# Performance work log

Hardware: AMD Instinct MI355X
Metric: run time of the kernel (lower is better)

## Reference

```python
import jax, jax.numpy as jnp
import numpy as np

N = 50000          # total residues (nodes)
E = 800000         # contact edges, avg degree 16
F_IN = 1280        # ESM embedding dim
H = 256            # hidden
L = 4              # num_layers
B = 100            # proteins in batch
MAX_NODES = 500    # residues per protein (uniform -> static to_dense_batch shape)


def setup_inputs() -> dict:
    key = jax.random.key(0)
    ks = jax.random.split(key, 16)
    s = 0.02
    inp = {
        "seq": jax.random.randint(ks[0], (N,), 0, 26),
        "edge_index": jax.random.randint(ks[1], (2, E), 0, N),
        "esm_token": jax.random.normal(ks[2], (N, F_IN), jnp.float32),
        "batch": jnp.arange(N) // MAX_NODES,
        # lin0
        "lin0_W": jax.random.normal(ks[3], (F_IN, H), jnp.float32) * s,
        "lin0_b": jnp.zeros((H,), jnp.float32),
        # WeightConv1 per layer: lin1 (root), lin2 (neighbor), lin3 (mask head)
        "wc_W1": jax.random.normal(ks[4], (L, H, H), jnp.float32) * s,
        "wc_b1": jnp.zeros((L, H), jnp.float32),
        "wc_W2": jax.random.normal(ks[5], (L, H, H), jnp.float32) * s,
        "wc_b2": jnp.zeros((L, H), jnp.float32),
        "wc_W3": jax.random.normal(ks[6], (L, H, H), jnp.float32) * s,
        "wc_b3": jnp.zeros((L, H), jnp.float32),
        # SparseConv per layer: neighbor weight + bias, root weight
        "sc_Wn": jax.random.normal(ks[7], (L, H, H), jnp.float32) * s,
        "sc_bn": jnp.zeros((L, H), jnp.float32),
        "sc_Wr": jax.random.normal(ks[8], (L, H, H), jnp.float32) * s,
    }
    return inp


def reference(seq, edge_index, esm_token, batch,
              lin0_W, lin0_b,
              wc_W1, wc_b1, wc_W2, wc_b2, wc_W3, wc_b3,
              sc_Wn, sc_bn, sc_Wr):
    src, dst = edge_index[0], edge_index[1]
    x = esm_token @ lin0_W + lin0_b              # [N, H]
    mask_val = None
    xs = []
    for i in range(L):
        # ---- WeightConv1: learned edge-conditioned node mask ----
        xm = x if mask_val is None else x * mask_val
        h_nb = xm @ wc_W2[i] + wc_b2[i]          # neighbor transform [N, H]
        agg = jax.ops.segment_sum(h_nb[src], dst, num_segments=N)
        h = jax.nn.relu(agg + xm @ wc_W1[i] + wc_b1[i])
        mask_val = jax.nn.sigmoid(h @ wc_W3[i] + wc_b3[i])   # [N, H]
        # ---- SparseConv: mask-gated sparse aggregation ----
        xg = x * mask_val
        agg2 = jax.ops.segment_sum(xg[src], dst, num_segments=N)
        x = jax.nn.relu(agg2 @ sc_Wn[i] + sc_bn[i] + x @ sc_Wr[i])
        xs.append(x)
    feat = jnp.concatenate(xs, axis=-1)          # jumping-knowledge cat [N, L*H]
    # ---- to_dense_batch ----
    counts = jax.ops.segment_sum(jnp.ones((N,), jnp.int32), batch, num_segments=B)
    starts = jnp.cumsum(counts) - counts
    pos = jnp.arange(N) - starts[batch]
    dense = jnp.zeros((B, MAX_NODES, L * H), feat.dtype).at[batch, pos].set(feat)
    node_mask = jnp.zeros((B, MAX_NODES), bool).at[batch, pos].set(True)
    return dense, node_mask
```

## Files before the change

### kernel.cpp

```cpp
#include <hip/hip_runtime.h>

#define NNODES 50000
#define HDIM 256
#define NLAYERS 4
#define NEDGES 800000
#define FIN 1280
#define LDOUT 1024

typedef _Float16 f16;
typedef __attribute__((ext_vector_type(8))) _Float16 f16x8;
typedef __attribute__((ext_vector_type(4))) _Float16 f16x4;
typedef __attribute__((ext_vector_type(4))) float f32x4;

enum { SRC_F32Y = 0, SRC_H = 1, SRC_MULH = 2, SRC_ADDRELU_H = 3, SRC_CATH = 4 };
enum { EPI_PART = 0, EPI_W2W1H = 1, EPI_MASKXG = 2, EPI_CATH = 3 };

template<int SRC, int EPI, int KTILES>
__global__ __launch_bounds__(256) void mgemm_k(
    const float* __restrict__ A1, int lda1,
    const f16*  __restrict__ A3,
    const f16*  __restrict__ A5,
    const f16*  __restrict__ A4,
    const f16*  __restrict__ Xh,
    const f16*  __restrict__ Wt,
    const f16*  __restrict__ Wt2,
    const float* __restrict__ bias,
    const float* __restrict__ bias2,
    float* __restrict__ Cf, int ldc,
    float* __restrict__ Cf2,
    f16*  __restrict__ Ch,
    f16*  __restrict__ Ch2)
{
    constexpr int K = KTILES * 64;
    __shared__ f16 Asm[2][4096];

    const int row0 = blockIdx.x * 64;
    const int by = blockIdx.y;
    const int tid = threadIdx.x;
    const int wv = tid >> 6;
    const int l = tid & 63;

    f32x4 acc[4][4] = {};

    const int sr = tid >> 2;
    const int sc0 = (tid & 3) * 16;
    const int grow = row0 + sr;
    const bool rok = grow < NNODES;
    const int kg = (SRC == SRC_F32Y) ? by * K : 0;
    const int lane_base0 =
        (((sc0 >> 5) * 4 + (sr >> 4)) * 64 + (sr & 15) + (((sc0 & 31) >> 3) * 16)) * 8;
    const int lane_base1 = lane_base0 + 128;

    const f16* Wsel = by ? Wt2 : Wt;
    const f16* bp[4];
    #pragma unroll
    for (int cf = 0; cf < 4; ++cf)
        bp[cf] = Wsel + (size_t)(wv * 64 + cf * 16 + (l & 15)) * K + ((l >> 4) * 8);

    struct SReg { float4 f0, f1, f2, f3; f16x8 h0, h1, g0, g1; };
    SReg RA, RB;

    auto LOAD = [&](SReg& r, int kt) {
        if (!rok) return;
        const int k0 = kt * 64 + sc0;
        if constexpr (SRC == SRC_F32Y) {
            const float* p = A1 + (size_t)grow * lda1 + kg + k0;
            r.f0 = *(const float4*)(p + 0);  r.f1 = *(const float4*)(p + 4);
            r.f2 = *(const float4*)(p + 8);  r.f3 = *(const float4*)(p + 12);
        } else if constexpr (SRC == SRC_H) {
            const f16* p = A3 + (size_t)grow * HDIM + k0;
            r.h0 = *(const f16x8*)p;  r.h1 = *(const f16x8*)(p + 8);
        } else if constexpr (SRC == SRC_MULH) {
            const f16* p = A3 + (size_t)grow * HDIM + k0;
            const f16* q = A5 + (size_t)grow * HDIM + k0;
            r.h0 = *(const f16x8*)p;  r.h1 = *(const f16x8*)(p + 8);
            r.g0 = *(const f16x8*)q;  r.g1 = *(const f16x8*)(q + 8);
        } else if constexpr (SRC == SRC_ADDRELU_H) {
            const float* p = A1 + (size_t)grow * HDIM + k0;
            const f16* q = A5 + (size_t)grow * HDIM + k0;
            r.f0 = *(const float4*)(p + 0);  r.f1 = *(const float4*)(p + 4);
            r.f2 = *(const float4*)(p + 8);  r.f3 = *(const float4*)(p + 12);
            r.h0 = *(const f16x8*)q;  r.h1 = *(const f16x8*)(q + 8);
        } else {
            const f16* p = (k0 < HDIM)
                ? (A3 + (size_t)grow * HDIM + k0)
                : (A4 + (size_t)grow * HDIM + (k0 - HDIM));
            r.h0 = *(const f16x8*)p;  r.h1 = *(const f16x8*)(p + 8);
        }
    };

    auto COMMIT = [&](const SReg& r, int b) {
        f16x8 av0, av1;
        #pragma unroll
        for (int i = 0; i < 8; ++i) { av0[i] = (f16)0.f; av1[i] = (f16)0.f; }
        if (rok) {
            if constexpr (SRC == SRC_F32Y) {
                av0[0]=(f16)r.f0.x; av0[1]=(f16)r.f0.y; av0[2]=(f16)r.f0.z; av0[3]=(f16)r.f0.w;
                av0[4]=(f16)r.f1.x; av0[5]=(f16)r.f1.y; av0[6]=(f16)r.f1.z; av0[7]=(f16)r.f1.w;
                av1[0]=(f16)r.f2.x; av1[1]=(f16)r.f2.y; av1[2]=(f16)r.f2.z; av1[3]=(f16)r.f2.w;
                av1[4]=(f16)r.f3.x; av1[5]=(f16)r.f3.y; av1[6]=(f16)r.f3.z; av1[7]=(f16)r.f3.w;
            } else if constexpr (SRC == SRC_H || SRC == SRC_CATH) {
                av0 = r.h0; av1 = r.h1;
            } else if constexpr (SRC == SRC_MULH) {
                #pragma unroll
                for (int i = 0; i < 8; ++i) {
                    av0[i] = (f16)((float)r.h0[i] * (float)r.g0[i]);
                    av1[i] = (f16)((float)r.h1[i] * (float)r.g1[i]);
                }
            } else if constexpr (SRC == SRC_ADDRELU_H) {
                av0[0]=(f16)fmaxf(r.f0.x+(float)r.h0[0],0.f); av0[1]=(f16)fmaxf(r.f0.y+(float)r.h0[1],0.f);
                av0[2]=(f16)fmaxf(r.f0.z+(float)r.h0[2],0.f); av0[3]=(f16)fmaxf(r.f0.w+(float)r.h0[3],0.f);
                av0[4]=(f16)fmaxf(r.f1.x+(float)r.h0[4],0.f); av0[5]=(f16)fmaxf(r.f1.y+(float)r.h0[5],0.f);
                av0[6]=(f16)fmaxf(r.f1.z+(float)r.h0[6],0.f); av0[7]=(f16)fmaxf(r.f1.w+(float)r.h0[7],0.f);
                av1[0]=(f16)fmaxf(r.f2.x+(float)r.h1[0],0.f); av1[1]=(f16)fmaxf(r.f2.y+(float)r.h1[1],0.f);
                av1[2]=(f16)fmaxf(r.f2.z+(float)r.h1[2],0.f); av1[3]=(f16)fmaxf(r.f2.w+(float)r.h1[3],0.f);
                av1[4]=(f16)fmaxf(r.f3.x+(float)r.h1[4],0.f); av1[5]=(f16)fmaxf(r.f3.y+(float)r.h1[5],0.f);
                av1[6]=(f16)fmaxf(r.f3.z+(float)r.h1[6],0.f); av1[7]=(f16)fmaxf(r.f3.w+(float)r.h1[7],0.f);
            }
        }
        *(f16x8*)(&Asm[b][lane_base0]) = av0;
        *(f16x8*)(&Asm[b][lane_base1]) = av1;
    };

    auto TILE = [&](int b, int kt) {
        f16x8 af[4][2];
        #pragma unroll
        for (int rf = 0; rf < 4; ++rf)
            #pragma unroll
            for (int kb = 0; kb < 2; ++kb)
                af[rf][kb] = *(const f16x8*)(&Asm[b][((kb * 4 + rf) * 64 + l) * 8]);
        f16x8 bfr[4][2];
        #pragma unroll
        for (int cf = 0; cf < 4; ++cf) {
            bfr[cf][0] = *(const f16x8*)(bp[cf] + kt * 64);
            bfr[cf][1] = *(const f16x8*)(bp[cf] + kt * 64 + 32);
        }
        #pragma unroll
        for (int cf = 0; cf < 4; ++cf)
            #pragma unroll
            for (int rf = 0; rf < 4; ++rf)
                #pragma unroll
                for (int kb = 0; kb < 2; ++kb)
                    acc[rf][cf] = __builtin_amdgcn_mfma_f32_16x16x32_f16(
                        af[rf][kb], bfr[cf][kb], acc[rf][cf], 0, 0, 0);
    };

    LOAD(RA, 0);
    COMMIT(RA, 0);
    if (KTILES > 1) LOAD(RB, 1);
    #pragma unroll
    for (int kt2 = 0; kt2 < KTILES; kt2 += 2) {
        __syncthreads();
        TILE(0, kt2);
        if (kt2 + 1 < KTILES) COMMIT(RB, 1);
        if (kt2 + 2 < KTILES) LOAD(RA, kt2 + 2);
        if (kt2 + 1 < KTILES) {
            __syncthreads();
            TILE(1, kt2 + 1);
            if (kt2 + 2 < KTILES) COMMIT(RA, 0);
            if (kt2 + 3 < KTILES) LOAD(RB, kt2 + 3);
        }
    }

    #pragma unroll
    for (int rf = 0; rf < 4; ++rf) {
        #pragma unroll
        for (int j = 0; j < 4; ++j) {
            const int row = row0 + rf * 16 + ((l >> 4) * 4) + j;
            if (row >= NNODES) continue;
            #pragma unroll
            for (int cf = 0; cf < 4; ++cf) {
                const int col = wv * 64 + cf * 16 + (l & 15);
                float v = acc[rf][cf][j];
                if constexpr (EPI == EPI_PART) {
                    (by ? Cf2 : Cf)[(size_t)row * HDIM + col] = v;
                } else if constexpr (EPI == EPI_W2W1H) {
                    if (by == 0) Ch[(size_t)row * HDIM + col]  = (f16)(v + bias[col]);
                    else         Ch2[(size_t)row * HDIM + col] = (f16)(v + bias2[col]);
                } else if constexpr (EPI == EPI_MASKXG) {
                    const float m = 1.f / (1.f + expf(-(v + bias[col])));
                    Ch2[(size_t)row * HDIM + col] = (f16)m;
                    Ch[(size_t)row * HDIM + col] =
                        (f16)((float)Xh[(size_t)row * HDIM + col] * m);
                } else {
                    const float r = fmaxf(v + bias[col], 0.f);
                    Cf[(size_t)row * ldc + col] = r;
                    Ch[(size_t)row * HDIM + col] = (f16)r;
                }
            }
        }
    }
}

__global__ __launch_bounds__(256) void combine_k(
    const float* __restrict__ P0, const float* __restrict__ P1,
    const float* __restrict__ b, f16* __restrict__ xh)
{
    const int t = blockIdx.x * 256 + threadIdx.x;
    const int row = t >> 6;
    const int c = (t & 63) * 4;
    if (row >= NNODES) return;
    const float4 a = *(const float4*)(P0 + (size_t)row * HDIM + c);
    const float4 d = *(const float4*)(P1 + (size_t)row * HDIM + c);
    const float4 bb = *(const float4*)(b + c);
    f16x4 r;
    r[0] = (f16)(a.x + d.x + bb.x); r[1] = (f16)(a.y + d.y + bb.y);
    r[2] = (f16)(a.z + d.z + bb.z); r[3] = (f16)(a.w + d.w + bb.w);
    *(f16x4*)(xh + (size_t)row * HDIM + c) = r;
}

__global__ __launch_bounds__(256) void pack_t_k(
    const float* __restrict__ W, f16* __restrict__ Wt, int K)
{
    const int idx = blockIdx.x * 256 + threadIdx.x;
    if (idx >= 256 * K) return;
    const int col = idx / K, k = idx % K;
    Wt[idx] = (f16)W[k * 256 + col];
}

__global__ __launch_bounds__(256) void pack_cat_k(
    const float* __restrict__ Wn, const float* __restrict__ Wr,
    f16* __restrict__ Wt)
{
    const int idx = blockIdx.x * 256 + threadIdx.x;
    if (idx >= 256 * 512) return;
    const int col = idx / 512, k = idx % 512;
    Wt[idx] = (f16)(k < 256 ? Wn[k * 256 + col] : Wr[(k - 256) * 256 + col]);
}

__global__ __launch_bounds__(256) void count_k(
    const int* __restrict__ dstIdx, int* __restrict__ counts)
{
    const int e = blockIdx.x * 256 + threadIdx.x;
    if (e < NEDGES) atomicAdd(&counts[dstIdx[e]], 1);
}

__global__ __launch_bounds__(1024) void scan_k(
    const int* __restrict__ counts, int* __restrict__ starts)
{
    __shared__ int sm[1024];
    __shared__ int s_off;
    if (threadIdx.x == 0) s_off = 0;
    __syncthreads();
    for (int base = 0; base < NNODES; base += 1024) {
        const int i = base + threadIdx.x;
        const int v = (i < NNODES) ? counts[i] : 0;
        sm[threadIdx.x] = v;
        __syncthreads();
        for (int ofs = 1; ofs < 1024; ofs <<= 1) {
            const int t = (threadIdx.x >= ofs) ? sm[threadIdx.x - ofs] : 0;
            __syncthreads();
            sm[threadIdx.x] += t;
            __syncthreads();
        }
        const int incl = sm[threadIdx.x];
        const int off = s_off;
        if (i < NNODES) starts[i] = off + incl - v;
        __syncthreads();
        if (threadIdx.x == 1023) s_off = off + incl;
        __syncthreads();
    }
    if (threadIdx.x == 0) starts[NNODES] = s_off;
}

__global__ __launch_bounds__(256) void fillcsr_k(
    const int* __restrict__ srcIdx, const int* __restrict__ dstIdx,
    int* __restrict__ cursor, int* __restrict__ csr)
{
    const int e = blockIdx.x * 256 + threadIdx.x;
    if (e >= NEDGES) return;
    const int d = dstIdx[e];
    const int p = atomicAdd(&cursor[d], 1);
    csr[p] = srcIdx[e];
}

__global__ __launch_bounds__(256) void gather_h_k(
    const f16* __restrict__ rows, const int* __restrict__ csr,
    const int* __restrict__ starts, float* __restrict__ outp)
{
    const int node = (blockIdx.x * 256 + threadIdx.x) >> 6;
    const int lane = threadIdx.x & 63;
    if (node >= NNODES) return;
    const int e0 = starts[node], e1 = starts[node + 1];
    float a0=0,a1=0,a2=0,a3=0, b0=0,b1=0,b2=0,b3=0;
    int e = e0;
    for (; e + 3 < e1; e += 4) {
        const int s0=csr[e], s1=csr[e+1], s2=csr[e+2], s3=csr[e+3];
        f16x4 v0 = *(const f16x4*)(rows + (size_t)s0 * HDIM + lane * 4);
        f16x4 v1 = *(const f16x4*)(rows + (size_t)s1 * HDIM + lane * 4);
        f16x4 v2 = *(const f16x4*)(rows + (size_t)s2 * HDIM + lane * 4);
        f16x4 v3 = *(const f16x4*)(rows + (size_t)s3 * HDIM + lane * 4);
        a0 += (float)v0[0] + (float)v2[0]; a1 += (float)v0[1] + (float)v2[1];
        a2 += (float)v0[2] + (float)v2[2]; a3 += (float)v0[3] + (float)v2[3];
        b0 += (float)v1[0] + (float)v3[0]; b1 += (float)v1[1] + (float)v3[1];
        b2 += (float)v1[2] + (float)v3[2]; b3 += (float)v1[3] + (float)v3[3];
    }
    for (; e < e1; ++e) {
        const int s0 = csr[e];
        f16x4 v0 = *(const f16x4*)(rows + (size_t)s0 * HDIM + lane * 4);
        a0 += (float)v0[0]; a1 += (float)v0[1]; a2 += (float)v0[2]; a3 += (float)v0[3];
    }
    *(float4*)(outp + (size_t)node * HDIM + lane * 4) =
        make_float4(a0 + b0, a1 + b1, a2 + b2, a3 + b3);
}

__global__ __launch_bounds__(256) void gather_g_k(
    const f16* __restrict__ rows, const int* __restrict__ csr,
    const int* __restrict__ starts, f16* __restrict__ outp)
{
    const int node = (blockIdx.x * 256 + threadIdx.x) >> 6;
    const int lane = threadIdx.x & 63;
    if (node >= NNODES) return;
    const int e0 = starts[node], e1 = starts[node + 1];
    float a0=0,a1=0,a2=0,a3=0, b0=0,b1=0,b2=0,b3=0;
    int e = e0;
    for (; e + 3 < e1; e += 4) {
        const int s0=csr[e], s1=csr[e+1], s2=csr[e+2], s3=csr[e+3];
        f16x4 v0 = *(const f16x4*)(rows + (size_t)s0 * HDIM + lane * 4);
        f16x4 v1 = *(const f16x4*)(rows + (size_t)s1 * HDIM + lane * 4);
        f16x4 v2 = *(const f16x4*)(rows + (size_t)s2 * HDIM + lane * 4);
        f16x4 v3 = *(const f16x4*)(rows + (size_t)s3 * HDIM + lane * 4);
        a0 += (float)v0[0] + (float)v2[0]; a1 += (float)v0[1] + (float)v2[1];
        a2 += (float)v0[2] + (float)v2[2]; a3 += (float)v0[3] + (float)v2[3];
        b0 += (float)v1[0] + (float)v3[0]; b1 += (float)v1[1] + (float)v3[1];
        b2 += (float)v1[2] + (float)v3[2]; b3 += (float)v1[3] + (float)v3[3];
    }
    for (; e < e1; ++e) {
        const int s0 = csr[e];
        f16x4 v0 = *(const f16x4*)(rows + (size_t)s0 * HDIM + lane * 4);
        a0 += (float)v0[0]; a1 += (float)v0[1]; a2 += (float)v0[2]; a3 += (float)v0[3];
    }
    f16x4 r;
    r[0] = (f16)(a0 + b0); r[1] = (f16)(a1 + b1);
    r[2] = (f16)(a2 + b2); r[3] = (f16)(a3 + b3);
    *(f16x4*)(outp + (size_t)node * HDIM + lane * 4) = r;
}

__global__ __launch_bounds__(256) void fill1_k(float* __restrict__ p, int n)
{
    const int t = blockIdx.x * 256 + threadIdx.x;
    if (t < n) p[t] = 1.0f;
}

extern "C" void kernel_launch(void* const* d_in, const int* in_sizes, int n_in,
                              void* d_out, int out_size, void* d_ws, size_t ws_size,
                              hipStream_t stream)
{
    const int*   edge   = (const int*)d_in[1];
    const int*   src    = edge;
    const int*   dst    = edge + NEDGES;
    const float* esm    = (const float*)d_in[2];
    const float* lin0_W = (const float*)d_in[4];
    const float* lin0_b = (const float*)d_in[5];
    const float* wc_W1  = (const float*)d_in[6];
    const float* wc_b1  = (const float*)d_in[7];
    const float* wc_W2  = (const float*)d_in[8];
    const float* wc_b2  = (const float*)d_in[9];
    const float* wc_W3  = (const float*)d_in[10];
    const float* wc_b3  = (const float*)d_in[11];
    const float* sc_Wn  = (const float*)d_in[12];
    const float* sc_bn  = (const float*)d_in[13];
    const float* sc_Wr  = (const float*)d_in[14];
    float* out = (float*)d_out;

    const size_t NH = (size_t)NNODES * HDIM;
    float* ws    = (float*)d_ws;
    float* aggf  = ws;
    float* part1 = ws + NH;
    f16*   xh    = (f16*)(ws + 2 * NH);
    f16*   hnb   = xh + NH;
    f16*   agg2  = hnb + NH;
    f16*   xw1h  = agg2 + NH;
    f16*   maskh = xw1h + NH;
    f16*   lin0tA = maskh + NH;
    f16*   lin0tB = lin0tA + 256 * 640;
    f16*   W2t   = lin0tB + 256 * 640;
    f16*   W1t   = W2t + 4 * 65536;
    f16*   W3t   = W1t + 4 * 65536;
    f16*   WtC   = W3t + 4 * 65536;
    int*   iws    = (int*)(WtC + 4 * 131072);
    int*   counts = iws;
    int*   starts = iws + NNODES;
    int*   cursor = iws + 2 * NNODES + 1;
    int*   csr    = iws + 3 * NNODES + 2;

    const dim3 blk(256);
    const int gemmGrid = (NNODES + 63) / 64;
    const int edgeGrid = (NEDGES + 255) / 256;
    const int waveGrid = (NNODES * 64) / 256;

    hipMemsetAsync(counts, 0, NNODES * sizeof(int), stream);
    count_k<<<edgeGrid, blk, 0, stream>>>(dst, counts);
    scan_k<<<1, 1024, 0, stream>>>(counts, starts);
    hipMemcpyAsync(cursor, starts, NNODES * sizeof(int),
                   hipMemcpyDeviceToDevice, stream);
    fillcsr_k<<<edgeGrid, blk, 0, stream>>>(src, dst, cursor, csr);

    pack_t_k<<<640, blk, 0, stream>>>(lin0_W, lin0tA, 640);
    pack_t_k<<<640, blk, 0, stream>>>(lin0_W + 640 * 256, lin0tB, 640);
    for (int i = 0; i < NLAYERS; ++i) {
        const size_t wo = (size_t)i * HDIM * HDIM;
        pack_t_k<<<256, blk, 0, stream>>>(wc_W2 + wo, W2t + i * 65536, 256);
        pack_t_k<<<256, blk, 0, stream>>>(wc_W1 + wo, W1t + i * 65536, 256);
        pack_t_k<<<256, blk, 0, stream>>>(wc_W3 + wo, W3t + i * 65536, 256);
        pack_cat_k<<<512, blk, 0, stream>>>(sc_Wn + wo, sc_Wr + wo, WtC + i * 131072);
    }

    mgemm_k<SRC_F32Y, EPI_PART, 10><<<dim3(gemmGrid, 2), blk, 0, stream>>>(
        esm, FIN, nullptr, nullptr, nullptr, nullptr, lin0tA, lin0tB,
        nullptr, nullptr, aggf, HDIM, part1, nullptr, nullptr);
    combine_k<<<waveGrid, blk, 0, stream>>>(aggf, part1, lin0_b, xh);

    for (int i = 0; i < NLAYERS; ++i) {
        const size_t bo = (size_t)i * HDIM;
        const f16* w2 = W2t + i * 65536;
        const f16* w1 = W1t + i * 65536;
        const f16* w3 = W3t + i * 65536;
        const f16* wc = WtC + i * 131072;

        if (i == 0) {
            mgemm_k<SRC_H, EPI_W2W1H, 4><<<dim3(gemmGrid, 2), blk, 0, stream>>>(
                nullptr, 0, xh, nullptr, nullptr, nullptr, w2, w1,
                wc_b2 + bo, wc_b1 + bo, nullptr, 0, nullptr, hnb, xw1h);
        } else {
            mgemm_k<SRC_MULH, EPI_W2W1H, 4><<<dim3(gemmGrid, 2), blk, 0, stream>>>(
                nullptr, 0, xh, maskh, nullptr, nullptr, w2, w1,
                wc_b2 + bo, wc_b1 + bo, nullptr, 0, nullptr, hnb, xw1h);
        }
        gather_h_k<<<waveGrid, blk, 0, stream>>>(hnb, csr, starts, aggf);
        mgemm_k<SRC_ADDRELU_H, EPI_MASKXG, 4><<<gemmGrid, blk, 0, stream>>>(
            aggf, HDIM, nullptr, xw1h, nullptr, xh, w3, w3,
            wc_b3 + bo, nullptr, nullptr, 0, nullptr, hnb, maskh);
        gather_g_k<<<waveGrid, blk, 0, stream>>>(hnb, csr, starts, agg2);
        mgemm_k<SRC_CATH, EPI_CATH, 8><<<gemmGrid, blk, 0, stream>>>(
            nullptr, 0, agg2, nullptr, xh, nullptr, wc, wc,
            sc_bn + bo, nullptr, out + (size_t)i * HDIM, LDOUT, nullptr, xh, nullptr);
    }

    const size_t maskOff = (size_t)NNODES * LDOUT;
    fill1_k<<<(NNODES + 255) / 256, blk, 0, stream>>>(out + maskOff, NNODES);
}
```

Baseline: 1.437 ms.

## Replace LDS-staged layer GEMMs with direct-register MFMA kernel and batch weight packing

The per-layer GEMMs (K=256/512) now use a new kernel in which each wave loads its A fragments straight from global memory into registers and issues 16x16x32 MFMAs over a 16x128 output tile. The grid doubles along columns, so there is no shared-memory staging and no __syncthreads. The many small weight-transpose launches are merged into one pack kernel. x is ping-ponged between two buffers so the last GEMM no longer overwrites its own input in place. The cost is more redundant global reads of A per output tile and less data reuse.

```diff
diff --git a/kernel.cpp b/kernel.cpp
--- a/kernel.cpp
+++ b/kernel.cpp
@@ -12,12 +12,12 @@
 typedef __attribute__((ext_vector_type(4))) _Float16 f16x4;
 typedef __attribute__((ext_vector_type(4))) float f32x4;
 
-enum { SRC_F32Y = 0, SRC_H = 1, SRC_MULH = 2, SRC_ADDRELU_H = 3, SRC_CATH = 4 };
-enum { EPI_PART = 0, EPI_W2W1H = 1, EPI_MASKXG = 2, EPI_CATH = 3 };
+enum { DSRC_H = 0, DSRC_MULH = 1, DSRC_ADDRELU = 2, DSRC_CATH = 3 };
+enum { DEPI_W2W1H = 0, DEPI_MASKXG = 1, DEPI_CATH = 2 };
 
 template<int SRC, int EPI, int KTILES>
-__global__ __launch_bounds__(256) void mgemm_k(
-    const float* __restrict__ A1, int lda1,
+__global__ __launch_bounds__(256) void dgemm_k(
+    const float* __restrict__ A1,
     const f16*  __restrict__ A3,
     const f16*  __restrict__ A5,
     const f16*  __restrict__ A4,
@@ -27,9 +27,117 @@
     const float* __restrict__ bias,
     const float* __restrict__ bias2,
     float* __restrict__ Cf, int ldc,
-    float* __restrict__ Cf2,
     f16*  __restrict__ Ch,
     f16*  __restrict__ Ch2)
+{
+    constexpr int K = KTILES * 32;
+    const int tid = threadIdx.x;
+    const int l = tid & 63;
+    const int wv = tid >> 6;
+    const int row0 = blockIdx.x * 64 + wv * 16;
+    if (row0 >= NNODES) return;
+    const int by = blockIdx.y;
+    const int col0 = (by & 1) * 128;
+    const int wsel = by >> 1;
+
+    const int arow = row0 + (l & 15);
+    const int ak = (l >> 4) * 8;
+
+    const f16* Wb = (EPI == DEPI_W2W1H && wsel) ? Wt2 : Wt;
+    const f16* bp[8];
+    #pragma unroll
+    for (int cf = 0; cf < 8; ++cf)
+        bp[cf] = Wb + (size_t)(col0 + cf * 16 + (l & 15)) * K + ak;
+
+    f32x4 acc[8] = {};
+
+    auto LOADA = [&](int kt) -> f16x8 {
+        const int k0 = kt * 32 + ak;
+        if constexpr (SRC == DSRC_H) {
+            return *(const f16x8*)(A3 + (size_t)arow * HDIM + k0);
+        } else if constexpr (SRC == DSRC_MULH) {
+            f16x8 h = *(const f16x8*)(A3 + (size_t)arow * HDIM + k0);
+            f16x8 m = *(const f16x8*)(A5 + (size_t)arow * HDIM + k0);
+            f16x8 r;
+            #pragma unroll
+            for (int i = 0; i < 8; ++i)
+                r[i] = (f16)((float)h[i] * (float)m[i]);
+            return r;
+        } else if constexpr (SRC == DSRC_ADDRELU) {
+            const float* p = A1 + (size_t)arow * HDIM + k0;
+            float4 a0 = *(const float4*)(p);
+            float4 a1 = *(const float4*)(p + 4);
+            f16x8 w = *(const f16x8*)(A5 + (size_t)arow * HDIM + k0);
+            f16x8 r;
+            r[0] = (f16)fmaxf(a0.x + (float)w[0], 0.f);
+            r[1] = (f16)fmaxf(a0.y + (float)w[1], 0.f);
+            r[2] = (f16)fmaxf(a0.z + (float)w[2], 0.f);
+            r[3] = (f16)fmaxf(a0.w + (float)w[3], 0.f);
+            r[4] = (f16)fmaxf(a1.x + (float)w[4], 0.f);
+            r[5] = (f16)fmaxf(a1.y + (float)w[5], 0.f);
+            r[6] = (f16)fmaxf(a1.z + (float)w[6], 0.f);
+            r[7] = (f16)fmaxf(a1.w + (float)w[7], 0.f);
+            return r;
+        } else {
+            if (kt < 8) return *(const f16x8*)(A3 + (size_t)arow * HDIM + kt * 32 + ak);
+            else        return *(const f16x8*)(A4 + (size_t)arow * HDIM + (kt - 8) * 32 + ak);
+        }
+    };
+
+    f16x8 aC = LOADA(0);
+    f16x8 bC[8];
+    #pragma unroll
+    for (int cf = 0; cf < 8; ++cf) bC[cf] = *(const f16x8*)(bp[cf]);
+
+    #pragma unroll
+    for (int kt = 0; kt < KTILES; ++kt) {
+        f16x8 aN;
+        f16x8 bN[8];
+        if (kt + 1 < KTILES) {
+            aN = LOADA(kt + 1);
+            #pragma unroll
+            for (int cf = 0; cf < 8; ++cf)
+                bN[cf] = *(const f16x8*)(bp[cf] + (kt + 1) * 32);
+        }
+        #pragma unroll
+        for (int cf = 0; cf < 8; ++cf)
+            acc[cf] = __builtin_amdgcn_mfma_f32_16x16x32_f16(aC, bC[cf], acc[cf], 0, 0, 0);
+        if (kt + 1 < KTILES) {
+            aC = aN;
+            #pragma unroll
+            for (int cf = 0; cf < 8; ++cf) bC[cf] = bN[cf];
+        }
+    }
+
+    #pragma unroll
+    for (int j = 0; j < 4; ++j) {
+        const int row = row0 + (l >> 4) * 4 + j;
+        #pragma unroll
+        for (int cf = 0; cf < 8; ++cf) {
+            const int col = col0 + cf * 16 + (l & 15);
+            float v = acc[cf][j];
+            if constexpr (EPI == DEPI_W2W1H) {
+                if (wsel == 0) Ch[(size_t)row * HDIM + col]  = (f16)(v + bias[col]);
+                else           Ch2[(size_t)row * HDIM + col] = (f16)(v + bias2[col]);
+            } else if constexpr (EPI == DEPI_MASKXG) {
+                const float m = 1.f / (1.f + expf(-(v + bias[col])));
+                Ch2[(size_t)row * HDIM + col] = (f16)m;
+                Ch[(size_t)row * HDIM + col] =
+                    (f16)((float)Xh[(size_t)row * HDIM + col] * m);
+            } else {
+                const float r = fmaxf(v + bias[col], 0.f);
+                Cf[(size_t)row * ldc + col] = r;
+                Ch[(size_t)row * HDIM + col] = (f16)r;
+            }
+        }
+    }
+}
+
+template<int KTILES>
+__global__ __launch_bounds__(256) void lin0_k(
+    const float* __restrict__ A1, int lda1,
+    const f16*  __restrict__ WtA, const f16* __restrict__ WtB,
+    float* __restrict__ Cf, float* __restrict__ Cf2)
 {
     constexpr int K = KTILES * 64;
     __shared__ f16 Asm[2][4096];
@@ -46,47 +154,25 @@
     const int sc0 = (tid & 3) * 16;
     const int grow = row0 + sr;
     const bool rok = grow < NNODES;
-    const int kg = (SRC == SRC_F32Y) ? by * K : 0;
+    const int kg = by * K;
     const int lane_base0 =
         (((sc0 >> 5) * 4 + (sr >> 4)) * 64 + (sr & 15) + (((sc0 & 31) >> 3) * 16)) * 8;
     const int lane_base1 = lane_base0 + 128;
 
-    const f16* Wsel = by ? Wt2 : Wt;
+    const f16* Wsel = by ? WtB : WtA;
     const f16* bp[4];
     #pragma unroll
     for (int cf = 0; cf < 4; ++cf)
         bp[cf] = Wsel + (size_t)(wv * 64 + cf * 16 + (l & 15)) * K + ((l >> 4) * 8);
 
-    struct SReg { float4 f0, f1, f2, f3; f16x8 h0, h1, g0, g1; };
+    struct SReg { float4 f0, f1, f2, f3; };
     SReg RA, RB;
 
     auto LOAD = [&](SReg& r, int kt) {
         if (!rok) return;
-        const int k0 = kt * 64 + sc0;
-        if constexpr (SRC == SRC_F32Y) {
-            const float* p = A1 + (size_t)grow * lda1 + kg + k0;
-            r.f0 = *(const float4*)(p + 0);  r.f1 = *(const float4*)(p + 4);
-            r.f2 = *(const float4*)(p + 8);  r.f3 = *(const float4*)(p + 12);
-        } else if constexpr (SRC == SRC_H) {
-            const f16* p = A3 + (size_t)grow * HDIM + k0;
-            r.h0 = *(const f16x8*)p;  r.h1 = *(const f16x8*)(p + 8);
-        } else if constexpr (SRC == SRC_MULH) {
-            const f16* p = A3 + (size_t)grow * HDIM + k0;
-            const f16* q = A5 + (size_t)grow * HDIM + k0;
-            r.h0 = *(const f16x8*)p;  r.h1 = *(const f16x8*)(p + 8);
-            r.g0 = *(const f16x8*)q;  r.g1 = *(const f16x8*)(q + 8);
-        } else if constexpr (SRC == SRC_ADDRELU_H) {
-            const float* p = A1 + (size_t)grow * HDIM + k0;
-            const f16* q = A5 + (size_t)grow * HDIM + k0;
-            r.f0 = *(const float4*)(p + 0);  r.f1 = *(const float4*)(p + 4);
-            r.f2 = *(const float4*)(p + 8);  r.f3 = *(const float4*)(p + 12);
-            r.h0 = *(const f16x8*)q;  r.h1 = *(const f16x8*)(q + 8);
-        } else {
-            const f16* p = (k0 < HDIM)
-                ? (A3 + (size_t)grow * HDIM + k0)
-                : (A4 + (size_t)grow * HDIM + (k0 - HDIM));
-            r.h0 = *(const f16x8*)p;  r.h1 = *(const f16x8*)(p + 8);
-        }
+        const float* p = A1 + (size_t)grow * lda1 + kg + kt * 64 + sc0;
+        r.f0 = *(const float4*)(p + 0);  r.f1 = *(const float4*)(p + 4);
+        r.f2 = *(const float4*)(p + 8);  r.f3 = *(const float4*)(p + 12);
     };
 
     auto COMMIT = [&](const SReg& r, int b) {
@@ -94,29 +180,10 @@
         #pragma unroll
         for (int i = 0; i < 8; ++i) { av0[i] = (f16)0.f; av1[i] = (f16)0.f; }
         if (rok) {
-            if constexpr (SRC == SRC_F32Y) {
-                av0[0]=(f16)r.f0.x; av0[1]=(f16)r.f0.y; av0[2]=(f16)r.f0.z; av0[3]=(f16)r.f0.w;
-                av0[4]=(f16)r.f1.x; av0[5]=(f16)r.f1.y; av0[6]=(f16)r.f1.z; av0[7]=(f16)r.f1.w;
-                av1[0]=(f16)r.f2.x; av1[1]=(f16)r.f2.y; av1[2]=(f16)r.f2.z; av1[3]=(f16)r.f2.w;
-                av1[4]=(f16)r.f3.x; av1[5]=(f16)r.f3.y; av1[6]=(f16)r.f3.z; av1[7]=(f16)r.f3.w;
-            } else if constexpr (SRC == SRC_H || SRC == SRC_CATH) {
-                av0 = r.h0; av1 = r.h1;
-            } else if constexpr (SRC == SRC_MULH) {
-                #pragma unroll
-                for (int i = 0; i < 8; ++i) {
-                    av0[i] = (f16)((float)r.h0[i] * (float)r.g0[i]);
-                    av1[i] = (f16)((float)r.h1[i] * (float)r.g1[i]);
-                }
-            } else if constexpr (SRC == SRC_ADDRELU_H) {
-                av0[0]=(f16)fmaxf(r.f0.x+(float)r.h0[0],0.f); av0[1]=(f16)fmaxf(r.f0.y+(float)r.h0[1],0.f);
-                av0[2]=(f16)fmaxf(r.f0.z+(float)r.h0[2],0.f); av0[3]=(f16)fmaxf(r.f0.w+(float)r.h0[3],0.f);
-                av0[4]=(f16)fmaxf(r.f1.x+(float)r.h0[4],0.f); av0[5]=(f16)fmaxf(r.f1.y+(float)r.h0[5],0.f);
-                av0[6]=(f16)fmaxf(r.f1.z+(float)r.h0[6],0.f); av0[7]=(f16)fmaxf(r.f1.w+(float)r.h0[7],0.f);
-                av1[0]=(f16)fmaxf(r.f2.x+(float)r.h1[0],0.f); av1[1]=(f16)fmaxf(r.f2.y+(float)r.h1[1],0.f);
-                av1[2]=(f16)fmaxf(r.f2.z+(float)r.h1[2],0.f); av1[3]=(f16)fmaxf(r.f2.w+(float)r.h1[3],0.f);
-                av1[4]=(f16)fmaxf(r.f3.x+(float)r.h1[4],0.f); av1[5]=(f16)fmaxf(r.f3.y+(float)r.h1[5],0.f);
-                av1[6]=(f16)fmaxf(r.f3.z+(float)r.h1[6],0.f); av1[7]=(f16)fmaxf(r.f3.w+(float)r.h1[7],0.f);
-            }
+            av0[0]=(f16)r.f0.x; av0[1]=(f16)r.f0.y; av0[2]=(f16)r.f0.z; av0[3]=(f16)r.f0.w;
+            av0[4]=(f16)r.f1.x; av0[5]=(f16)r.f1.y; av0[6]=(f16)r.f1.z; av0[7]=(f16)r.f1.w;
+            av1[0]=(f16)r.f2.x; av1[1]=(f16)r.f2.y; av1[2]=(f16)r.f2.z; av1[3]=(f16)r.f2.w;
+            av1[4]=(f16)r.f3.x; av1[5]=(f16)r.f3.y; av1[6]=(f16)r.f3.z; av1[7]=(f16)r.f3.w;
         }
         *(f16x8*)(&Asm[b][lane_base0]) = av0;
         *(f16x8*)(&Asm[b][lane_base1]) = av1;
@@ -171,22 +238,7 @@
             #pragma unroll
             for (int cf = 0; cf < 4; ++cf) {
                 const int col = wv * 64 + cf * 16 + (l & 15);
-                float v = acc[rf][cf][j];
-                if constexpr (EPI == EPI_PART) {
-                    (by ? Cf2 : Cf)[(size_t)row * HDIM + col] = v;
-                } else if constexpr (EPI == EPI_W2W1H) {
-                    if (by == 0) Ch[(size_t)row * HDIM + col]  = (f16)(v + bias[col]);
-                    else         Ch2[(size_t)row * HDIM + col] = (f16)(v + bias2[col]);
-                } else if constexpr (EPI == EPI_MASKXG) {
-                    const float m = 1.f / (1.f + expf(-(v + bias[col])));
-                    Ch2[(size_t)row * HDIM + col] = (f16)m;
-                    Ch[(size_t)row * HDIM + col] =
-                        (f16)((float)Xh[(size_t)row * HDIM + col] * m);
-                } else {
-                    const float r = fmaxf(v + bias[col], 0.f);
-                    Cf[(size_t)row * ldc + col] = r;
-                    Ch[(size_t)row * HDIM + col] = (f16)r;
-                }
+                (by ? Cf2 : Cf)[(size_t)row * HDIM + col] = acc[rf][cf][j];
             }
         }
     }
@@ -209,23 +261,39 @@
     *(f16x4*)(xh + (size_t)row * HDIM + c) = r;
 }
 
-__global__ __launch_bounds__(256) void pack_t_k(
-    const float* __restrict__ W, f16* __restrict__ Wt, int K)
-{
-    const int idx = blockIdx.x * 256 + threadIdx.x;
-    if (idx >= 256 * K) return;
-    const int col = idx / K, k = idx % K;
-    Wt[idx] = (f16)W[k * 256 + col];
-}
-
-__global__ __launch_bounds__(256) void pack_cat_k(
+__global__ __launch_bounds__(256) void pack_all_k(
+    const float* __restrict__ lin0_W,
+    const float* __restrict__ W2, const float* __restrict__ W1,
+    const float* __restrict__ W3,
     const float* __restrict__ Wn, const float* __restrict__ Wr,
-    f16* __restrict__ Wt)
-{
-    const int idx = blockIdx.x * 256 + threadIdx.x;
-    if (idx >= 256 * 512) return;
-    const int col = idx / 512, k = idx % 512;
-    Wt[idx] = (f16)(k < 256 ? Wn[k * 256 + col] : Wr[(k - 256) * 256 + col]);
+    f16* __restrict__ dst)
+{
+    int idx = blockIdx.x * 256 + threadIdx.x;
+    const int total = 163840 * 2 + 262144 * 3 + 524288;
+    if (idx >= total) return;
+    f16* d = dst + idx;
+    if (idx < 327680) {
+        const int half = idx / 163840;
+        int r = idx % 163840;
+        const int col = r / 640, k = r % 640;
+        *d = (f16)lin0_W[(size_t)(k + half * 640) * 256 + col];
+        return;
+    }
+    idx -= 327680;
+    if (idx < 786432) {
+        const int which = idx / 262144;
+        int r = idx % 262144;
+        const int i = r / 65536; r %= 65536;
+        const int col = r / 256, k = r % 256;
+        const float* W = (which == 0) ? W2 : (which == 1) ? W1 : W3;
+        *d = (f16)W[(size_t)i * 65536 + k * 256 + col];
+        return;
+    }
+    idx -= 786432;
+    const int i = idx / 131072; int r = idx % 131072;
+    const int col = r / 512, k = r % 512;
+    *d = (f16)(k < 256 ? Wn[(size_t)i * 65536 + k * 256 + col]
+                       : Wr[(size_t)i * 65536 + (k - 256) * 256 + col]);
 }
 
 __global__ __launch_bounds__(256) void count_k(
@@ -367,18 +435,20 @@
     float* ws    = (float*)d_ws;
     float* aggf  = ws;
     float* part1 = ws + NH;
-    f16*   xh    = (f16*)(ws + 2 * NH);
-    f16*   hnb   = xh + NH;
+    f16*   xhA   = (f16*)(ws + 2 * NH);
+    f16*   xhB   = xhA + NH;
+    f16*   hnb   = xhB + NH;
     f16*   agg2  = hnb + NH;
     f16*   xw1h  = agg2 + NH;
     f16*   maskh = xw1h + NH;
-    f16*   lin0tA = maskh + NH;
-    f16*   lin0tB = lin0tA + 256 * 640;
-    f16*   W2t   = lin0tB + 256 * 640;
-    f16*   W1t   = W2t + 4 * 65536;
-    f16*   W3t   = W1t + 4 * 65536;
-    f16*   WtC   = W3t + 4 * 65536;
-    int*   iws    = (int*)(WtC + 4 * 131072);
+    f16*   wpack = maskh + NH;
+    f16*   lin0tA = wpack;
+    f16*   lin0tB = lin0tA + 163840;
+    f16*   W2t   = lin0tB + 163840;
+    f16*   W1t   = W2t + 262144;
+    f16*   W3t   = W1t + 262144;
+    f16*   WtC   = W3t + 262144;
+    int*   iws    = (int*)(WtC + 524288);
     int*   counts = iws;
     int*   starts = iws + NNODES;
     int*   cursor = iws + 2 * NNODES + 1;
@@ -396,20 +466,12 @@
                    hipMemcpyDeviceToDevice, stream);
     fillcsr_k<<<edgeGrid, blk, 0, stream>>>(src, dst, cursor, csr);
 
-    pack_t_k<<<640, blk, 0, stream>>>(lin0_W, lin0tA, 640);
-    pack_t_k<<<640, blk, 0, stream>>>(lin0_W + 640 * 256, lin0tB, 640);
-    for (int i = 0; i < NLAYERS; ++i) {
-        const size_t wo = (size_t)i * HDIM * HDIM;
-        pack_t_k<<<256, blk, 0, stream>>>(wc_W2 + wo, W2t + i * 65536, 256);
-        pack_t_k<<<256, blk, 0, stream>>>(wc_W1 + wo, W1t + i * 65536, 256);
-        pack_t_k<<<256, blk, 0, stream>>>(wc_W3 + wo, W3t + i * 65536, 256);
-        pack_cat_k<<<512, blk, 0, stream>>>(sc_Wn + wo, sc_Wr + wo, WtC + i * 131072);
-    }
-
-    mgemm_k<SRC_F32Y, EPI_PART, 10><<<dim3(gemmGrid, 2), blk, 0, stream>>>(
-        esm, FIN, nullptr, nullptr, nullptr, nullptr, lin0tA, lin0tB,
-        nullptr, nullptr, aggf, HDIM, part1, nullptr, nullptr);
-    combine_k<<<waveGrid, blk, 0, stream>>>(aggf, part1, lin0_b, xh);
+    pack_all_k<<<(1638400 + 255) / 256, blk, 0, stream>>>(
+        lin0_W, wc_W2, wc_W1, wc_W3, sc_Wn, sc_Wr, wpack);
+
+    lin0_k<10><<<dim3(gemmGrid, 2), blk, 0, stream>>>(
+        esm, FIN, lin0tA, lin0tB, aggf, part1);
+    combine_k<<<waveGrid, blk, 0, stream>>>(aggf, part1, lin0_b, xhA);
 
     for (int i = 0; i < NLAYERS; ++i) {
         const size_t bo = (size_t)i * HDIM;
@@ -417,24 +479,26 @@
         const f16* w1 = W1t + i * 65536;
         const f16* w3 = W3t + i * 65536;
         const f16* wc = WtC + i * 131072;
+        const f16* xcur = (i & 1) ? xhB : xhA;
+        f16*       xnew = (i & 1) ? xhA : xhB;
 
         if (i == 0) {
-            mgemm_k<SRC_H, EPI_W2W1H, 4><<<dim3(gemmGrid, 2), blk, 0, stream>>>(
-                nullptr, 0, xh, nullptr, nullptr, nullptr, w2, w1,
-                wc_b2 + bo, wc_b1 + bo, nullptr, 0, nullptr, hnb, xw1h);
+            dgemm_k<DSRC_H, DEPI_W2W1H, 8><<<dim3(gemmGrid, 4), blk, 0, stream>>>(
+                nullptr, xcur, nullptr, nullptr, nullptr, w2, w1,
+                wc_b2 + bo, wc_b1 + bo, nullptr, 0, hnb, xw1h);
         } else {
-            mgemm_k<SRC_MULH, EPI_W2W1H, 4><<<dim3(gemmGrid, 2), blk, 0, stream>>>(
-                nullptr, 0, xh, maskh, nullptr, nullptr, w2, w1,
-                wc_b2 + bo, wc_b1 + bo, nullptr, 0, nullptr, hnb, xw1h);
+            dgemm_k<DSRC_MULH, DEPI_W2W1H, 8><<<dim3(gemmGrid, 4), blk, 0, stream>>>(
+                nullptr, xcur, maskh, nullptr, nullptr, w2, w1,
+                wc_b2 + bo, wc_b1 + bo, nullptr, 0, hnb, xw1h);
         }
         gather_h_k<<<waveGrid, blk, 0, stream>>>(hnb, csr, starts, aggf);
-        mgemm_k<SRC_ADDRELU_H, EPI_MASKXG, 4><<<gemmGrid, blk, 0, stream>>>(
-            aggf, HDIM, nullptr, xw1h, nullptr, xh, w3, w3,
-            wc_b3 + bo, nullptr, nullptr, 0, nullptr, hnb, maskh);
+        dgemm_k<DSRC_ADDRELU, DEPI_MASKXG, 8><<<dim3(gemmGrid, 2), blk, 0, stream>>>(
+            aggf, nullptr, xw1h, nullptr, xcur, w3, nullptr,
+            wc_b3 + bo, nullptr, nullptr, 0, hnb, maskh);
         gather_g_k<<<waveGrid, blk, 0, stream>>>(hnb, csr, starts, agg2);
-        mgemm_k<SRC_CATH, EPI_CATH, 8><<<gemmGrid, blk, 0, stream>>>(
-            nullptr, 0, agg2, nullptr, xh, nullptr, wc, wc,
-            sc_bn + bo, nullptr, out + (size_t)i * HDIM, LDOUT, nullptr, xh, nullptr);
+        dgemm_k<DSRC_CATH, DEPI_CATH, 16><<<dim3(gemmGrid, 2), blk, 0, stream>>>(
+            nullptr, agg2, nullptr, xcur, nullptr, wc, nullptr,
+            sc_bn + bo, nullptr, out + (size_t)i * HDIM, LDOUT, xnew, nullptr);
     }
 
     const size_t maskOff = (size_t)NNODES * LDOUT;
```

Result: slower. 2.072 ms (+44.2%).
